# Kernel tuning notes

Hardware: AMD Instinct MI355X
Metric: run time of the kernel (lower is better)

## Reference

```python
import jax, jax.numpy as jnp
import numpy as np

N, T, H, D, E, P, R = 50000, 16, 512, 256, 200000, 100000, 3
LN_EPS = 1e-5
BN_EPS = 1e-5


def setup_inputs() -> dict:
    key = jax.random.key(0)
    ks = jax.random.split(key, 32)
    ri = lambda k, shape, hi: jax.random.randint(k, shape, 0, hi)
    rn = lambda k, shape, scale=0.05: (jax.random.normal(k, shape, dtype=jnp.float32) * scale)
    return {
        "node_type_ids": ri(ks[0], (N,), T),
        "src0": ri(ks[1], (E,), N), "dst0": ri(ks[2], (E,), N),
        "src1": ri(ks[3], (E,), N), "dst1": ri(ks[4], (E,), N),
        "src2": ri(ks[5], (E,), N), "dst2": ri(ks[6], (E,), N),
        "pairs": ri(ks[7], (2, P), N),
        "degrees": ri(ks[8], (N,), 100),
        "node_emb": rn(ks[9], (N, H)),
        "type_emb": rn(ks[10], (T, H)),
        "w_loop_in": rn(ks[11], (H, H)),
        "w_rel_in": rn(ks[12], (R, H, H)),
        "w_loop_res": rn(ks[13], (H, H)),
        "w_rel_res": rn(ks[14], (R, H, H)),
        "ln_g": jnp.ones((H,), jnp.float32),
        "ln_b": jnp.zeros((H,), jnp.float32),
        "w_loop_out": rn(ks[15], (H, D)),
        "w_rel_out": rn(ks[16], (R, H, D)),
        "lp_w1": rn(ks[17], (3 * D, D)),
        "lp_b1": jnp.zeros((D,), jnp.float32),
        "bn_g": jnp.ones((D,), jnp.float32),
        "bn_b": jnp.zeros((D,), jnp.float32),
        "bn_mean": jnp.zeros((D,), jnp.float32),
        "bn_var": jnp.ones((D,), jnp.float32),
        "lp_w2": rn(ks[18], (D, 1)),
        "lp_b2": jnp.zeros((1,), jnp.float32),
        "alpha": jnp.float32(0.1),
        "beta": jnp.float32(0.1),
    }


def _rgcn(x, loop_w, rel_w, srcs, dsts):
    # out = x @ W_loop + sum_r (A_r @ x) @ W_r ; A_r unweighted COO -> segment_sum
    out = x @ loop_w
    for r in range(R):
        msg = jax.ops.segment_sum(x[srcs[r]], dsts[r], num_segments=x.shape[0])
        out = out + msg @ rel_w[r]
    return out


def _layernorm(h, g, b):
    mu = h.mean(-1, keepdims=True)
    var = h.var(-1, keepdims=True)
    return (h - mu) * jax.lax.rsqrt(var + LN_EPS) * g + b


def reference(node_type_ids, src0, dst0, src1, dst1, src2, dst2, pairs, degrees,
              node_emb, type_emb, w_loop_in, w_rel_in, w_loop_res, w_rel_res,
              ln_g, ln_b, w_loop_out, w_rel_out, lp_w1, lp_b1, bn_g, bn_b,
              bn_mean, bn_var, lp_w2, lp_b2, alpha, beta):
    srcs = (src0, src1, src2)
    dsts = (dst0, dst1, dst2)
    # encode
    x = node_emb + type_emb[node_type_ids]          # [N, H]
    x = jax.nn.relu(_rgcn(x, w_loop_in, w_rel_in, srcs, dsts))
    h = _rgcn(x, w_loop_res, w_rel_res, srcs, dsts)
    h = jax.nn.relu(_layernorm(h, ln_g, ln_b))      # dropout p=0 -> identity
    x = x + h
    z = _rgcn(x, w_loop_out, w_rel_out, srcs, dsts)  # [N, D]
    # score
    src_z = z[pairs[0]]                              # [P, D]
    dst_z = z[pairs[1]]
    src_deg = jnp.clip(degrees[pairs[0]], 1).astype(jnp.float32)
    dst_deg = jnp.clip(degrees[pairs[1]], 1).astype(jnp.float32)
    feats = jnp.concatenate([src_z, dst_z, src_z * dst_z], axis=-1)  # [P, 3D]
    h1 = jax.nn.relu(feats @ lp_w1 + lp_b1)
    # BatchNorm1d in eval mode: running stats
    h1 = (h1 - bn_mean) * jax.lax.rsqrt(bn_var + BN_EPS) * bn_g + bn_b
    mlp_score = (h1 @ lp_w2 + lp_b2).squeeze(-1)     # [P]
    base = mlp_score - jax.nn.relu(alpha) * jnp.log(src_deg) - jax.nn.relu(beta) * jnp.log(dst_deg)
    return base / (jnp.sqrt(src_deg) * jnp.sqrt(dst_deg) + 1e-8)
```

## Files before the change

kernel.cpp:

```cpp
#include <hip/hip_runtime.h>

typedef __attribute__((ext_vector_type(8))) _Float16 half8;
typedef __attribute__((ext_vector_type(4))) _Float16 half4;
typedef __attribute__((ext_vector_type(4))) float f32x4;

static __device__ __forceinline__ void gload16(const void* g, void* l) {
  __builtin_amdgcn_global_load_lds((const __attribute__((address_space(1))) void*)g,
                                   (__attribute__((address_space(3))) void*)l, 16, 0, 0);
}

__global__ void k_encode(const float* __restrict__ emb, const float* __restrict__ temb,
                         const int* __restrict__ tids, _Float16* __restrict__ x, int n) {
  int i = blockIdx.x * 256 + threadIdx.x;
  if (i >= n * 64) return;
  int node = i >> 6, c = (i & 63) << 3;
  const float* e = emb + (size_t)node * 512 + c;
  const float* t = temb + (size_t)tids[node] * 512 + c;
  float4 a0 = *(const float4*)e, a1 = *(const float4*)(e + 4);
  float4 b0 = *(const float4*)t, b1 = *(const float4*)(t + 4);
  half8 o;
  o[0] = (_Float16)(a0.x + b0.x); o[1] = (_Float16)(a0.y + b0.y);
  o[2] = (_Float16)(a0.z + b0.z); o[3] = (_Float16)(a0.w + b0.w);
  o[4] = (_Float16)(a1.x + b1.x); o[5] = (_Float16)(a1.y + b1.y);
  o[6] = (_Float16)(a1.z + b1.z); o[7] = (_Float16)(a1.w + b1.w);
  *(half8*)(x + (size_t)node * 512 + c) = o;
}

__global__ void k_zero(int* __restrict__ p, int n) {
  int i = blockIdx.x * 256 + threadIdx.x;
  if (i < n) p[i] = 0;
}

__global__ void k_hist(const int* __restrict__ d0, const int* __restrict__ d1,
                       const int* __restrict__ d2, int* __restrict__ counts, int E, int Np1) {
  int e = blockIdx.x * 256 + threadIdx.x;
  if (e >= E) return;
  int r = blockIdx.y;
  const int* d = (r == 0) ? d0 : ((r == 1) ? d1 : d2);
  atomicAdd(&counts[r * Np1 + d[e] + 1], 1);
}

__global__ void k_scan(const int* __restrict__ counts, int* __restrict__ rowp, int n) {
  __shared__ int wsum[16];
  int r = blockIdx.x;
  const int* c = counts + (size_t)r * n;
  int* o = rowp + (size_t)r * n;
  int lane = threadIdx.x & 63, w = threadIdx.x >> 6;
  int off = 0;
  for (int base = 0; base < n; base += 1024) {
    int i = base + threadIdx.x;
    int v = (i < n) ? c[i] : 0;
    int sc = v;
    #pragma unroll
    for (int d = 1; d < 64; d <<= 1) {
      int t = __shfl_up(sc, (unsigned)d);
      if (lane >= d) sc += t;
    }
    if (lane == 63) wsum[w] = sc;
    __syncthreads();
    int wo = 0, tot = 0;
    #pragma unroll
    for (int ww = 0; ww < 16; ++ww) {
      int s = wsum[ww];
      if (ww < w) wo += s;
      tot += s;
    }
    if (i < n) o[i] = sc + wo + off;
    off += tot;
    __syncthreads();
  }
}

__global__ void k_copy(const int* __restrict__ a, int* __restrict__ b, int n) {
  int i = blockIdx.x * 256 + threadIdx.x;
  if (i < n) b[i] = a[i];
}

__global__ void k_fill(const int* __restrict__ s0, const int* __restrict__ s1, const int* __restrict__ s2,
                       const int* __restrict__ d0, const int* __restrict__ d1, const int* __restrict__ d2,
                       int* __restrict__ cursor, int* __restrict__ col_src, int E, int Np1) {
  int e = blockIdx.x * 256 + threadIdx.x;
  if (e >= E) return;
  int r = blockIdx.y;
  const int* dp = (r == 0) ? d0 : ((r == 1) ? d1 : d2);
  const int* sp = (r == 0) ? s0 : ((r == 1) ? s1 : s2);
  int pos = atomicAdd(&cursor[r * Np1 + dp[e]], 1);
  if (pos >= 0 && pos < E) col_src[(size_t)r * E + pos] = sp[e];
}

__global__ void k_aggregate(const _Float16* __restrict__ x, _Float16* __restrict__ agg,
                            const int* __restrict__ rowp, const int* __restrict__ col_src,
                            int N, int E) {
  int wid = (blockIdx.x * 256 + threadIdx.x) >> 6;
  int lane = threadIdx.x & 63;
  if (wid >= N) return;
  int Np1 = N + 1;
  #pragma unroll
  for (int r = 0; r < 3; ++r) {
    int beg = rowp[r * Np1 + wid], end = rowp[r * Np1 + wid + 1];
    const int* cs = col_src + (size_t)r * E;
    float acc[8] = {0, 0, 0, 0, 0, 0, 0, 0};
    int sn = (beg < end) ? cs[beg] : 0;
    for (int e = beg; e < end; ++e) {
      int sc = sn;
      if (e + 1 < end) sn = cs[e + 1];
      half8 v = *(const half8*)(x + (size_t)sc * 512 + lane * 8);
      #pragma unroll
      for (int j = 0; j < 8; ++j) acc[j] += (float)v[j];
    }
    half8 o;
    #pragma unroll
    for (int j = 0; j < 8; ++j) o[j] = (_Float16)acc[j];
    *(half8*)(agg + (size_t)wid * 1536 + r * 512 + lane * 8) = o;
  }
}

__global__ void k_transpose_all(const float* __restrict__ wli, const float* __restrict__ wri,
                                const float* __restrict__ wlr, const float* __restrict__ wrr,
                                const float* __restrict__ wlo, const float* __restrict__ wro,
                                const float* __restrict__ lpw1,
                                _Float16* __restrict__ Bti, _Float16* __restrict__ Btr,
                                _Float16* __restrict__ Bto, _Float16* __restrict__ Btl) {
  __shared__ float tile[64][65];
  int zi = blockIdx.z;
  const float* Bl; const float* Br; _Float16* Bt; int No, K;
  if (zi == 0)      { Bl = wli;  Br = wri;            Bt = Bti; No = 512; K = 2048; }
  else if (zi == 1) { Bl = wlr;  Br = wrr;            Bt = Btr; No = 512; K = 2048; }
  else if (zi == 2) { Bl = wlo;  Br = wro;            Bt = Bto; No = 256; K = 2048; }
  else              { Bl = lpw1; Br = lpw1 + 512*256; Bt = Btl; No = 256; K = 768;  }
  int k0 = blockIdx.x * 64, n0 = blockIdx.y * 64;
  if (k0 >= K || n0 >= No) return;
  int nl = threadIdx.x & 63, kb = threadIdx.x >> 6;
  #pragma unroll
  for (int i = 0; i < 16; ++i) {
    int kl = kb + i * 4;
    int krow = k0 + kl;
    float v = (krow < 512) ? Bl[(size_t)krow * No + n0 + nl]
                           : Br[(size_t)(krow - 512) * No + n0 + nl];
    tile[kl][nl] = v;
  }
  __syncthreads();
  int kl = threadIdx.x & 63, nb = threadIdx.x >> 6;
  #pragma unroll
  for (int i = 0; i < 16; ++i) {
    int n2 = nb + i * 4;
    Bt[(size_t)(n0 + n2) * K + k0 + kl] = (_Float16)tile[kl][n2];
  }
}

__global__ __launch_bounds__(512) void k_gemm_rgcn(
    const _Float16* __restrict__ Ain, const _Float16* __restrict__ Aagg,
    const _Float16* __restrict__ Bt, _Float16* __restrict__ C,
    int M, int Ncols, int K, int relu, int S, int T) {
  __shared__ __align__(16) _Float16 As[256 * 64];
  __shared__ __align__(16) _Float16 Bs[128 * 64];
  int lin = blockIdx.x;
  int grp = lin / (8 * T);
  int rmd = lin - grp * 8 * T;
  int c = rmd >> 3, x = rmd & 7;
  int s = grp * 8 + x;
  if (s >= S) return;
  int bm0 = s * 256, bn0 = c * 128;

  int tid = threadIdx.x;
  int lane = tid & 63, wv = tid >> 6;
  int wm = wv & 3, wn = wv >> 2;
  int l16 = lane & 15, quad = lane >> 4;

  int rl8 = lane >> 3;
  int gs = (lane & 7) ^ rl8;

  int rA[4];
  const _Float16* pa[4];
  const _Float16* pb[2];
  _Float16* ldA[4];
  _Float16* ldB[2];
  #pragma unroll
  for (int q = 0; q < 4; ++q) {
    int chunk = wv * 4 + q;
    int rl = chunk * 8 + rl8;
    int ra = bm0 + rl; if (ra >= M) ra = M - 1;
    rA[q] = ra;
    pa[q] = Ain + (size_t)ra * 512 + gs * 8;
    ldA[q] = &As[chunk * 8 * 64];
  }
  #pragma unroll
  for (int q = 0; q < 2; ++q) {
    int chunk = wv * 2 + q;
    int rl = chunk * 8 + rl8;
    pb[q] = Bt + (size_t)(bn0 + rl) * K + gs * 8;
    ldB[q] = &Bs[chunk * 8 * 64];
  }

  f32x4 acc[4][4];
  #pragma unroll
  for (int i = 0; i < 4; ++i)
    #pragma unroll
    for (int j = 0; j < 4; ++j) acc[i][j] = (f32x4){0.f, 0.f, 0.f, 0.f};

  for (int k0 = 0; k0 < K; k0 += 64) {
    if (k0 == 512) {
      #pragma unroll
      for (int q = 0; q < 4; ++q) pa[q] = Aagg + (size_t)rA[q] * 1536 + gs * 8;
    }
    __syncthreads();
    #pragma unroll
    for (int q = 0; q < 4; ++q) gload16(pa[q], ldA[q]);
    #pragma unroll
    for (int q = 0; q < 2; ++q) gload16(pb[q], ldB[q]);
    __syncthreads();
    #pragma unroll
    for (int sb = 0; sb < 2; ++sb) {
      half8 af[4], bf[4];
      int slot = ((sb * 4 + quad) ^ (l16 & 7)) * 8;
      #pragma unroll
      for (int i = 0; i < 4; ++i)
        af[i] = *(const half8*)&As[(wm * 64 + i * 16 + l16) * 64 + slot];
      #pragma unroll
      for (int j = 0; j < 4; ++j)
        bf[j] = *(const half8*)&Bs[(wn * 64 + j * 16 + l16) * 64 + slot];
      #pragma unroll
      for (int i = 0; i < 4; ++i)
        #pragma unroll
        for (int j = 0; j < 4; ++j)
          acc[i][j] = __builtin_amdgcn_mfma_f32_16x16x32_f16(af[i], bf[j], acc[i][j], 0, 0, 0);
    }
    #pragma unroll
    for (int q = 0; q < 4; ++q) pa[q] += 64;
    #pragma unroll
    for (int q = 0; q < 2; ++q) pb[q] += 64;
  }

  #pragma unroll
  for (int i = 0; i < 4; ++i)
    #pragma unroll
    for (int j = 0; j < 4; ++j)
      #pragma unroll
      for (int rg = 0; rg < 4; ++rg) {
        int row = bm0 + wm * 64 + i * 16 + quad * 4 + rg;
        int col = bn0 + wn * 64 + j * 16 + l16;
        if (row < M) {
          float v = acc[i][j][rg];
          if (relu) v = fmaxf(v, 0.f);
          C[(size_t)row * Ncols + col] = (_Float16)v;
        }
      }
}

#define LSTR 40

__global__ __launch_bounds__(256) void k_gemm_link(
    const _Float16* __restrict__ z, const int* __restrict__ pairs,
    const _Float16* __restrict__ Bt,
    const float* __restrict__ b1, const float* __restrict__ bng, const float* __restrict__ bnb,
    const float* __restrict__ bnm, const float* __restrict__ bnv,
    _Float16* __restrict__ h1, int P, int K) {
  __shared__ __align__(16) _Float16 As[128 * LSTR];
  __shared__ __align__(16) _Float16 Bs[128 * LSTR];
  int tid = threadIdx.x;
  int bn0 = blockIdx.x * 128, bm0 = blockIdx.y * 128;
  int lane = tid & 63, wv = tid >> 6;
  int wm = wv & 1, wn = wv >> 1;
  int l16 = lane & 15, quad = lane >> 4;
  int srow = tid >> 1, scs = (tid & 1) * 16;
  int p = bm0 + srow; if (p >= P) p = P - 1;
  int sp = pairs[p], dp = pairs[P + p];
  const _Float16* zs = z + (size_t)sp * 256;
  const _Float16* zd = z + (size_t)dp * 256;
  int bgn = bn0 + srow;

  f32x4 acc[4][4];
  #pragma unroll
  for (int i = 0; i < 4; ++i)
    #pragma unroll
    for (int j = 0; j < 4; ++j) acc[i][j] = (f32x4){0.f, 0.f, 0.f, 0.f};

  for (int k0 = 0; k0 < K; k0 += 32) {
    __syncthreads();
    int seg = k0 >> 8;
    int kk = (k0 & 255) + scs;
    __attribute__((aligned(16))) _Float16 tmp[16];
    if (seg == 0) {
      *(uint4*)tmp = *(const uint4*)(zs + kk);
      *(uint4*)(tmp + 8) = *(const uint4*)(zs + kk + 8);
    } else if (seg == 1) {
      *(uint4*)tmp = *(const uint4*)(zd + kk);
      *(uint4*)(tmp + 8) = *(const uint4*)(zd + kk + 8);
    } else {
      half8 u0 = *(const half8*)(zs + kk), u1 = *(const half8*)(zs + kk + 8);
      half8 v0 = *(const half8*)(zd + kk), v1 = *(const half8*)(zd + kk + 8);
      #pragma unroll
      for (int j = 0; j < 8; ++j) {
        tmp[j] = (_Float16)((float)u0[j] * (float)v0[j]);
        tmp[j + 8] = (_Float16)((float)u1[j] * (float)v1[j]);
      }
    }
    *(uint4*)&As[srow * LSTR + scs] = *(const uint4*)tmp;
    *(uint4*)&As[srow * LSTR + scs + 8] = *(const uint4*)(tmp + 8);
    {
      const _Float16* src = Bt + (size_t)bgn * K + k0 + scs;
      *(uint4*)&Bs[srow * LSTR + scs] = *(const uint4*)src;
      *(uint4*)&Bs[srow * LSTR + scs + 8] = *(const uint4*)(src + 8);
    }
    __syncthreads();
    half8 af[4], bf[4];
    #pragma unroll
    for (int i = 0; i < 4; ++i)
      af[i] = *(const half8*)&As[(wm * 64 + i * 16 + l16) * LSTR + quad * 8];
    #pragma unroll
    for (int j = 0; j < 4; ++j)
      bf[j] = *(const half8*)&Bs[(wn * 64 + j * 16 + l16) * LSTR + quad * 8];
    #pragma unroll
    for (int i = 0; i < 4; ++i)
      #pragma unroll
      for (int j = 0; j < 4; ++j)
        acc[i][j] = __builtin_amdgcn_mfma_f32_16x16x32_f16(af[i], bf[j], acc[i][j], 0, 0, 0);
  }

  #pragma unroll
  for (int i = 0; i < 4; ++i)
    #pragma unroll
    for (int j = 0; j < 4; ++j) {
      int col = bn0 + wn * 64 + j * 16 + l16;
      float bb1 = b1[col], m = bnm[col], rs = rsqrtf(bnv[col] + 1e-5f);
      float gg = bng[col], bb = bnb[col];
      #pragma unroll
      for (int rg = 0; rg < 4; ++rg) {
        int row = bm0 + wm * 64 + i * 16 + quad * 4 + rg;
        if (row < P) {
          float v = fmaxf(acc[i][j][rg] + bb1, 0.f);
          v = (v - m) * rs * gg + bb;
          h1[(size_t)row * 256 + col] = (_Float16)v;
        }
      }
    }
}

__global__ void k_ln_res(const _Float16* __restrict__ h, const _Float16* __restrict__ x1,
                         const float* __restrict__ g, const float* __restrict__ b,
                         _Float16* __restrict__ out, int N) {
  int wid = (blockIdx.x * 256 + threadIdx.x) >> 6;
  int lane = threadIdx.x & 63;
  if (wid >= N) return;
  int c = lane * 8;
  half8 hv = *(const half8*)(h + (size_t)wid * 512 + c);
  float hf[8];
  float s = 0.f, sq = 0.f;
  #pragma unroll
  for (int j = 0; j < 8; ++j) {
    hf[j] = (float)hv[j];
    s += hf[j];
    sq += hf[j] * hf[j];
  }
  #pragma unroll
  for (int off = 32; off; off >>= 1) {
    s += __shfl_down(s, (unsigned)off);
    sq += __shfl_down(sq, (unsigned)off);
  }
  s = __shfl(s, 0); sq = __shfl(sq, 0);
  float mu = s * (1.f / 512.f);
  float var = sq * (1.f / 512.f) - mu * mu;
  float rs = rsqrtf(var + 1e-5f);
  float4 g0 = *(const float4*)(g + c), g1 = *(const float4*)(g + c + 4);
  float4 b0 = *(const float4*)(b + c), b1 = *(const float4*)(b + c + 4);
  float gf[8] = {g0.x, g0.y, g0.z, g0.w, g1.x, g1.y, g1.z, g1.w};
  float bf[8] = {b0.x, b0.y, b0.z, b0.w, b1.x, b1.y, b1.z, b1.w};
  half8 xv = *(const half8*)(x1 + (size_t)wid * 512 + c);
  half8 o;
  #pragma unroll
  for (int j = 0; j < 8; ++j) {
    float xw = (float)xv[j];
    o[j] = (_Float16)(xw + fmaxf((hf[j] - mu) * rs * gf[j] + bf[j], 0.f));
  }
  *(half8*)(out + (size_t)wid * 512 + c) = o;
}

__global__ void k_score(const _Float16* __restrict__ h1, const float* __restrict__ w2,
                        const float* __restrict__ b2, const int* __restrict__ pairs,
                        const int* __restrict__ degrees, const float* __restrict__ alpha,
                        const float* __restrict__ beta, float* __restrict__ out, int P) {
  int wid = (blockIdx.x * 256 + threadIdx.x) >> 6;
  int lane = threadIdx.x & 63;
  if (wid >= P) return;
  int c = lane * 4;
  half4 hv = *(const half4*)(h1 + (size_t)wid * 256 + c);
  float4 wv = *(const float4*)(w2 + c);
  float s = (float)hv[0] * wv.x + (float)hv[1] * wv.y + (float)hv[2] * wv.z + (float)hv[3] * wv.w;
  #pragma unroll
  for (int off = 32; off; off >>= 1) s += __shfl_down(s, (unsigned)off);
  if (lane == 0) {
    int sp = pairs[wid], dp = pairs[P + wid];
    float sd = (float)max(degrees[sp], 1);
    float dd = (float)max(degrees[dp], 1);
    float base = s + b2[0] - fmaxf(alpha[0], 0.f) * logf(sd) - fmaxf(beta[0], 0.f) * logf(dd);
    out[wid] = base / (sqrtf(sd) * sqrtf(dd) + 1e-8f);
  }
}

extern "C" void kernel_launch(void* const* d_in, const int* in_sizes, int n_in,
                              void* d_out, int out_size, void* d_ws, size_t ws_size,
                              hipStream_t stream) {
  const int N = 50000, E = 200000, P = 100000;
  const int Np1 = N + 1;
  const int* node_type = (const int*)d_in[0];
  const int* src0 = (const int*)d_in[1]; const int* dst0 = (const int*)d_in[2];
  const int* src1 = (const int*)d_in[3]; const int* dst1 = (const int*)d_in[4];
  const int* src2 = (const int*)d_in[5]; const int* dst2 = (const int*)d_in[6];
  const int* pairs = (const int*)d_in[7];
  const int* degrees = (const int*)d_in[8];
  const float* node_emb = (const float*)d_in[9];
  const float* type_emb = (const float*)d_in[10];
  const float* w_loop_in = (const float*)d_in[11];
  const float* w_rel_in = (const float*)d_in[12];
  const float* w_loop_res = (const float*)d_in[13];
  const float* w_rel_res = (const float*)d_in[14];
  const float* ln_g = (const float*)d_in[15];
  const float* ln_b = (const float*)d_in[16];
  const float* w_loop_out = (const float*)d_in[17];
  const float* w_rel_out = (const float*)d_in[18];
  const float* lp_w1 = (const float*)d_in[19];
  const float* lp_b1 = (const float*)d_in[20];
  const float* bn_g = (const float*)d_in[21];
  const float* bn_b = (const float*)d_in[22];
  const float* bn_mean = (const float*)d_in[23];
  const float* bn_var = (const float*)d_in[24];
  const float* lp_w2 = (const float*)d_in[25];
  const float* lp_b2 = (const float*)d_in[26];
  const float* alpha = (const float*)d_in[27];
  const float* beta = (const float*)d_in[28];
  float* out = (float*)d_out;

  char* ws = (char*)d_ws;
  size_t off = 0;
  auto alloc = [&](size_t bytes) {
    void* p = ws + off;
    off = (off + bytes + 255) & ~(size_t)255;
    return p;
  };
  _Float16* xb0 = (_Float16*)alloc((size_t)N * 512 * 2);
  _Float16* xb1 = (_Float16*)alloc((size_t)N * 512 * 2);
  _Float16* agg = (_Float16*)alloc((size_t)N * 1536 * 2);
  _Float16* Bti = (_Float16*)alloc((size_t)512 * 2048 * 2);
  _Float16* Btr = (_Float16*)alloc((size_t)512 * 2048 * 2);
  _Float16* Bto = (_Float16*)alloc((size_t)256 * 2048 * 2);
  _Float16* Btl = (_Float16*)alloc((size_t)256 * 768 * 2);
  int* counts = (int*)alloc((size_t)3 * Np1 * 4);
  int* rowp = (int*)alloc((size_t)3 * Np1 * 4);
  int* cursor = (int*)alloc((size_t)3 * Np1 * 4);
  int* col_src = (int*)alloc((size_t)3 * E * 4);
  if (off > ws_size) return;

  _Float16* z = xb1;
  _Float16* h1 = agg;

  k_transpose_all<<<dim3(32, 8, 4), 256, 0, stream>>>(
      w_loop_in, w_rel_in, w_loop_res, w_rel_res, w_loop_out, w_rel_out, lp_w1,
      Bti, Btr, Bto, Btl);

  k_zero<<<(3 * Np1 + 255) / 256, 256, 0, stream>>>(counts, 3 * Np1);
  dim3 gE((E + 255) / 256, 3);
  k_hist<<<gE, 256, 0, stream>>>(dst0, dst1, dst2, counts, E, Np1);
  k_scan<<<3, 1024, 0, stream>>>(counts, rowp, Np1);
  k_copy<<<(3 * Np1 + 255) / 256, 256, 0, stream>>>(rowp, cursor, 3 * Np1);
  k_fill<<<gE, 256, 0, stream>>>(src0, src1, src2, dst0, dst1, dst2, cursor, col_src, E, Np1);

  k_encode<<<(N * 64 + 255) / 256, 256, 0, stream>>>(node_emb, type_emb, node_type, xb0, N);

  int aggBlocks = (N + 3) / 4;
  const int S = (N + 255) / 256;
  int blocks4 = ((S + 7) / 8) * 8 * 4;
  int blocks2 = ((S + 7) / 8) * 8 * 2;

  k_aggregate<<<aggBlocks, 256, 0, stream>>>(xb0, agg, rowp, col_src, N, E);
  k_gemm_rgcn<<<blocks4, 512, 0, stream>>>(xb0, agg, Bti, xb1, N, 512, 2048, 1, S, 4);

  k_aggregate<<<aggBlocks, 256, 0, stream>>>(xb1, agg, rowp, col_src, N, E);
  k_gemm_rgcn<<<blocks4, 512, 0, stream>>>(xb1, agg, Btr, xb0, N, 512, 2048, 0, S, 4);

  k_ln_res<<<(N + 3) / 4, 256, 0, stream>>>(xb0, xb1, ln_g, ln_b, xb0, N);

  k_aggregate<<<aggBlocks, 256, 0, stream>>>(xb0, agg, rowp, col_src, N, E);
  k_gemm_rgcn<<<blocks2, 512, 0, stream>>>(xb0, agg, Bto, z, N, 256, 2048, 0, S, 2);

  dim3 gl(2, (P + 127) / 128);
  k_gemm_link<<<gl, 256, 0, stream>>>(z, pairs, Btl, lp_b1, bn_g, bn_b, bn_mean, bn_var, h1, P, 768);

  k_score<<<(P + 3) / 4, 256, 0, stream>>>(h1, lp_w2, lp_b2, pairs, degrees, alpha, beta, out, P);
}
```

Baseline: 1.058 ms.

## Materialize link features and use swizzled LDS-DMA GEMM; unroll aggregation gathers

The link-prediction GEMM is split in two. A new kernel first materializes the concatenated [src, dst, src*dst] features into a buffer. A second GEMM then loads tiles with global_load_lds into an XOR-swizzled 64-wide LDS layout, using 256x128 tiles, 512 threads and grouped block ordering. The per-node aggregation loop is also unrolled by 4 so several independent row gathers are in flight at once. The cost is an extra pass writing and reading the P x 768 feature buffer, and h1 now reuses xb0.

Result: slower. 1.093 ms (+3.3%).

```diff
diff --git a/kernel.cpp b/kernel.cpp
--- a/kernel.cpp
+++ b/kernel.cpp
@@ -95,23 +95,41 @@
   int lane = threadIdx.x & 63;
   if (wid >= N) return;
   int Np1 = N + 1;
+  int co = lane * 8;
   #pragma unroll
   for (int r = 0; r < 3; ++r) {
     int beg = rowp[r * Np1 + wid], end = rowp[r * Np1 + wid + 1];
     const int* cs = col_src + (size_t)r * E;
     float acc[8] = {0, 0, 0, 0, 0, 0, 0, 0};
-    int sn = (beg < end) ? cs[beg] : 0;
-    for (int e = beg; e < end; ++e) {
-      int sc = sn;
-      if (e + 1 < end) sn = cs[e + 1];
-      half8 v = *(const half8*)(x + (size_t)sc * 512 + lane * 8);
-      #pragma unroll
-      for (int j = 0; j < 8; ++j) acc[j] += (float)v[j];
+    int e = beg;
+    for (; e + 4 <= end; e += 4) {
+      int s0 = cs[e], s1 = cs[e + 1], s2 = cs[e + 2], s3 = cs[e + 3];
+      half8 v0 = *(const half8*)(x + (size_t)s0 * 512 + co);
+      half8 v1 = *(const half8*)(x + (size_t)s1 * 512 + co);
+      half8 v2 = *(const half8*)(x + (size_t)s2 * 512 + co);
+      half8 v3 = *(const half8*)(x + (size_t)s3 * 512 + co);
+      #pragma unroll
+      for (int j = 0; j < 8; ++j)
+        acc[j] += ((float)v0[j] + (float)v1[j]) + ((float)v2[j] + (float)v3[j]);
+    }
+    if (e + 2 <= end) {
+      int s0 = cs[e], s1 = cs[e + 1];
+      half8 v0 = *(const half8*)(x + (size_t)s0 * 512 + co);
+      half8 v1 = *(const half8*)(x + (size_t)s1 * 512 + co);
+      #pragma unroll
+      for (int j = 0; j < 8; ++j) acc[j] += (float)v0[j] + (float)v1[j];
+      e += 2;
+    }
+    if (e < end) {
+      int s0 = cs[e];
+      half8 v0 = *(const half8*)(x + (size_t)s0 * 512 + co);
+      #pragma unroll
+      for (int j = 0; j < 8; ++j) acc[j] += (float)v0[j];
     }
     half8 o;
     #pragma unroll
     for (int j = 0; j < 8; ++j) o[j] = (_Float16)acc[j];
-    *(half8*)(agg + (size_t)wid * 1536 + r * 512 + lane * 8) = o;
+    *(half8*)(agg + (size_t)wid * 1536 + r * 512 + co) = o;
   }
 }
 
@@ -247,27 +265,69 @@
       }
 }
 
-#define LSTR 40
-
-__global__ __launch_bounds__(256) void k_gemm_link(
-    const _Float16* __restrict__ z, const int* __restrict__ pairs,
-    const _Float16* __restrict__ Bt,
+__global__ void k_feats(const _Float16* __restrict__ z, const int* __restrict__ pairs,
+                        _Float16* __restrict__ feats, int P) {
+  unsigned int i = blockIdx.x * 256 + threadIdx.x;
+  if (i >= (unsigned)P * 96u) return;
+  unsigned int p = i / 96u;
+  int c8 = (int)(i - p * 96u);
+  int sp = pairs[p], dp = pairs[P + p];
+  half8 o;
+  if (c8 < 32) {
+    o = *(const half8*)(z + (size_t)sp * 256 + c8 * 8);
+  } else if (c8 < 64) {
+    o = *(const half8*)(z + (size_t)dp * 256 + (c8 - 32) * 8);
+  } else {
+    half8 u = *(const half8*)(z + (size_t)sp * 256 + (c8 - 64) * 8);
+    half8 v = *(const half8*)(z + (size_t)dp * 256 + (c8 - 64) * 8);
+    #pragma unroll
+    for (int j = 0; j < 8; ++j) o[j] = (_Float16)((float)u[j] * (float)v[j]);
+  }
+  *(half8*)(feats + (size_t)p * 768 + c8 * 8) = o;
+}
+
+__global__ __launch_bounds__(512) void k_gemm_linkB(
+    const _Float16* __restrict__ feats, const _Float16* __restrict__ Bt,
     const float* __restrict__ b1, const float* __restrict__ bng, const float* __restrict__ bnb,
     const float* __restrict__ bnm, const float* __restrict__ bnv,
-    _Float16* __restrict__ h1, int P, int K) {
-  __shared__ __align__(16) _Float16 As[128 * LSTR];
-  __shared__ __align__(16) _Float16 Bs[128 * LSTR];
+    _Float16* __restrict__ h1, int P, int K, int S, int T) {
+  __shared__ __align__(16) _Float16 As[256 * 64];
+  __shared__ __align__(16) _Float16 Bs[128 * 64];
+  int lin = blockIdx.x;
+  int grp = lin / (8 * T);
+  int rmd = lin - grp * 8 * T;
+  int c = rmd >> 3, x = rmd & 7;
+  int s = grp * 8 + x;
+  if (s >= S) return;
+  int bm0 = s * 256, bn0 = c * 128;
+
   int tid = threadIdx.x;
-  int bn0 = blockIdx.x * 128, bm0 = blockIdx.y * 128;
   int lane = tid & 63, wv = tid >> 6;
-  int wm = wv & 1, wn = wv >> 1;
+  int wm = wv & 3, wn = wv >> 2;
   int l16 = lane & 15, quad = lane >> 4;
-  int srow = tid >> 1, scs = (tid & 1) * 16;
-  int p = bm0 + srow; if (p >= P) p = P - 1;
-  int sp = pairs[p], dp = pairs[P + p];
-  const _Float16* zs = z + (size_t)sp * 256;
-  const _Float16* zd = z + (size_t)dp * 256;
-  int bgn = bn0 + srow;
+
+  int rl8 = lane >> 3;
+  int gs = (lane & 7) ^ rl8;
+
+  const _Float16* pa[4];
+  const _Float16* pb[2];
+  _Float16* ldA[4];
+  _Float16* ldB[2];
+  #pragma unroll
+  for (int q = 0; q < 4; ++q) {
+    int chunk = wv * 4 + q;
+    int rl = chunk * 8 + rl8;
+    int ra = bm0 + rl; if (ra >= P) ra = P - 1;
+    pa[q] = feats + (size_t)ra * 768 + gs * 8;
+    ldA[q] = &As[chunk * 8 * 64];
+  }
+  #pragma unroll
+  for (int q = 0; q < 2; ++q) {
+    int chunk = wv * 2 + q;
+    int rl = chunk * 8 + rl8;
+    pb[q] = Bt + (size_t)(bn0 + rl) * K + gs * 8;
+    ldB[q] = &Bs[chunk * 8 * 64];
+  }
 
   f32x4 acc[4][4];
   #pragma unroll
@@ -275,55 +335,42 @@
     #pragma unroll
     for (int j = 0; j < 4; ++j) acc[i][j] = (f32x4){0.f, 0.f, 0.f, 0.f};
 
-  for (int k0 = 0; k0 < K; k0 += 32) {
+  for (int k0 = 0; k0 < K; k0 += 64) {
     __syncthreads();
-    int seg = k0 >> 8;
-    int kk = (k0 & 255) + scs;
-    __attribute__((aligned(16))) _Float16 tmp[16];
-    if (seg == 0) {
-      *(uint4*)tmp = *(const uint4*)(zs + kk);
-      *(uint4*)(tmp + 8) = *(const uint4*)(zs + kk + 8);
-    } else if (seg == 1) {
-      *(uint4*)tmp = *(const uint4*)(zd + kk);
-      *(uint4*)(tmp + 8) = *(const uint4*)(zd + kk + 8);
-    } else {
-      half8 u0 = *(const half8*)(zs + kk), u1 = *(const half8*)(zs + kk + 8);
-      half8 v0 = *(const half8*)(zd + kk), v1 = *(const half8*)(zd + kk + 8);
-      #pragma unroll
-      for (int j = 0; j < 8; ++j) {
-        tmp[j] = (_Float16)((float)u0[j] * (float)v0[j]);
-        tmp[j + 8] = (_Float16)((float)u1[j] * (float)v1[j]);
-      }
-    }
-    *(uint4*)&As[srow * LSTR + scs] = *(const uint4*)tmp;
-    *(uint4*)&As[srow * LSTR + scs + 8] = *(const uint4*)(tmp + 8);
-    {
-      const _Float16* src = Bt + (size_t)bgn * K + k0 + scs;
-      *(uint4*)&Bs[srow * LSTR + scs] = *(const uint4*)src;
-      *(uint4*)&Bs[srow * LSTR + scs + 8] = *(const uint4*)(src + 8);
-    }
+    #pragma unroll
+    for (int q = 0; q < 4; ++q) gload16(pa[q], ldA[q]);
+    #pragma unroll
+    for (int q = 0; q < 2; ++q) gload16(pb[q], ldB[q]);
     __syncthreads();
-    half8 af[4], bf[4];
+    #pragma unroll
+    for (int sb = 0; sb < 2; ++sb) {
+      half8 af[4], bf[4];
+      int slot = ((sb * 4 + quad) ^ (l16 & 7)) * 8;
+      #pragma unroll
+      for (int i = 0; i < 4; ++i)
+        af[i] = *(const half8*)&As[(wm * 64 + i * 16 + l16) * 64 + slot];
+      #pragma unroll
+      for (int j = 0; j < 4; ++j)
+        bf[j] = *(const half8*)&Bs[(wn * 64 + j * 16 + l16) * 64 + slot];
+      #pragma unroll
+      for (int i = 0; i < 4; ++i)
+        #pragma unroll
+        for (int j = 0; j < 4; ++j)
+          acc[i][j] = __builtin_amdgcn_mfma_f32_16x16x32_f16(af[i], bf[j], acc[i][j], 0, 0, 0);
+    }
+    #pragma unroll
+    for (int q = 0; q < 4; ++q) pa[q] += 64;
+    #pragma unroll
+    for (int q = 0; q < 2; ++q) pb[q] += 64;
+  }
+
+  #pragma unroll
+  for (int j = 0; j < 4; ++j) {
+    int col = bn0 + wn * 64 + j * 16 + l16;
+    float bb1 = b1[col], m = bnm[col], rs = rsqrtf(bnv[col] + 1e-5f);
+    float gg = bng[col], bb = bnb[col];
     #pragma unroll
     for (int i = 0; i < 4; ++i)
-      af[i] = *(const half8*)&As[(wm * 64 + i * 16 + l16) * LSTR + quad * 8];
-    #pragma unroll
-    for (int j = 0; j < 4; ++j)
-      bf[j] = *(const half8*)&Bs[(wn * 64 + j * 16 + l16) * LSTR + quad * 8];
-    #pragma unroll
-    for (int i = 0; i < 4; ++i)
-      #pragma unroll
-      for (int j = 0; j < 4; ++j)
-        acc[i][j] = __builtin_amdgcn_mfma_f32_16x16x32_f16(af[i], bf[j], acc[i][j], 0, 0, 0);
-  }
-
-  #pragma unroll
-  for (int i = 0; i < 4; ++i)
-    #pragma unroll
-    for (int j = 0; j < 4; ++j) {
-      int col = bn0 + wn * 64 + j * 16 + l16;
-      float bb1 = b1[col], m = bnm[col], rs = rsqrtf(bnv[col] + 1e-5f);
-      float gg = bng[col], bb = bnb[col];
       #pragma unroll
       for (int rg = 0; rg < 4; ++rg) {
         int row = bm0 + wm * 64 + i * 16 + quad * 4 + rg;
@@ -333,7 +380,7 @@
           h1[(size_t)row * 256 + col] = (_Float16)v;
         }
       }
-    }
+  }
 }
 
 __global__ void k_ln_res(const _Float16* __restrict__ h, const _Float16* __restrict__ x1,
@@ -451,7 +498,8 @@
   if (off > ws_size) return;
 
   _Float16* z = xb1;
-  _Float16* h1 = agg;
+  _Float16* feats = agg;
+  _Float16* h1 = xb0;
 
   k_transpose_all<<<dim3(32, 8, 4), 256, 0, stream>>>(
       w_loop_in, w_rel_in, w_loop_res, w_rel_res, w_loop_out, w_rel_out, lp_w1,
@@ -482,8 +530,11 @@
   k_aggregate<<<aggBlocks, 256, 0, stream>>>(xb0, agg, rowp, col_src, N, E);
   k_gemm_rgcn<<<blocks2, 512, 0, stream>>>(xb0, agg, Bto, z, N, 256, 2048, 0, S, 2);
 
-  dim3 gl(2, (P + 127) / 128);
-  k_gemm_link<<<gl, 256, 0, stream>>>(z, pairs, Btl, lp_b1, bn_g, bn_b, bn_mean, bn_var, h1, P, 768);
+  k_feats<<<((unsigned)P * 96u + 255) / 256, 256, 0, stream>>>(z, pairs, feats, P);
+  const int SL = (P + 255) / 256;
+  int blocksL = ((SL + 7) / 8) * 8 * 2;
+  k_gemm_linkB<<<blocksL, 512, 0, stream>>>(feats, Btl, lp_b1, bn_g, bn_b, bn_mean, bn_var,
+                                            h1, P, 768, SL, 2);
 
   k_score<<<(P + 3) / 4, 256, 0, stream>>>(h1, lp_w2, lp_b2, pairs, degrees, alpha, beta, out, P);
 }
```

## Merge per-relation CSR into one combined CSR with relation-tagged columns

Applied to the files above, without the earlier changes.

Builds a single CSR over destination nodes holding all three relations, with the relation id packed into the top byte of each column index. The aggregate kernel then walks one edge list per node with 4-way unrolled gathers and branches to one of three accumulators. The zero and copy kernels are dropped: a memset clears the counts and the scan writes the cursor directly, cutting launches. The aim is more memory-level parallelism in the gather; the cost is data-dependent branching per edge and a node-id limit of 2^24.

Result: no change. 1.074 ms (+1.5%).

```diff
diff --git a/kernel.cpp b/kernel.cpp
--- a/kernel.cpp
+++ b/kernel.cpp
@@ -26,30 +26,23 @@
   *(half8*)(x + (size_t)node * 512 + c) = o;
 }
 
-__global__ void k_zero(int* __restrict__ p, int n) {
-  int i = blockIdx.x * 256 + threadIdx.x;
-  if (i < n) p[i] = 0;
-}
-
 __global__ void k_hist(const int* __restrict__ d0, const int* __restrict__ d1,
-                       const int* __restrict__ d2, int* __restrict__ counts, int E, int Np1) {
+                       const int* __restrict__ d2, int* __restrict__ counts, int E) {
   int e = blockIdx.x * 256 + threadIdx.x;
   if (e >= E) return;
   int r = blockIdx.y;
   const int* d = (r == 0) ? d0 : ((r == 1) ? d1 : d2);
-  atomicAdd(&counts[r * Np1 + d[e] + 1], 1);
-}
-
-__global__ void k_scan(const int* __restrict__ counts, int* __restrict__ rowp, int n) {
+  atomicAdd(&counts[d[e] + 1], 1);
+}
+
+__global__ void k_scan(const int* __restrict__ counts, int* __restrict__ rowp,
+                       int* __restrict__ cursor, int n) {
   __shared__ int wsum[16];
-  int r = blockIdx.x;
-  const int* c = counts + (size_t)r * n;
-  int* o = rowp + (size_t)r * n;
   int lane = threadIdx.x & 63, w = threadIdx.x >> 6;
   int off = 0;
   for (int base = 0; base < n; base += 1024) {
     int i = base + threadIdx.x;
-    int v = (i < n) ? c[i] : 0;
+    int v = (i < n) ? counts[i] : 0;
     int sc = v;
     #pragma unroll
     for (int d = 1; d < 64; d <<= 1) {
@@ -65,54 +58,82 @@
       if (ww < w) wo += s;
       tot += s;
     }
-    if (i < n) o[i] = sc + wo + off;
+    if (i < n) { int val = sc + wo + off; rowp[i] = val; cursor[i] = val; }
     off += tot;
     __syncthreads();
   }
 }
 
-__global__ void k_copy(const int* __restrict__ a, int* __restrict__ b, int n) {
-  int i = blockIdx.x * 256 + threadIdx.x;
-  if (i < n) b[i] = a[i];
-}
-
 __global__ void k_fill(const int* __restrict__ s0, const int* __restrict__ s1, const int* __restrict__ s2,
                        const int* __restrict__ d0, const int* __restrict__ d1, const int* __restrict__ d2,
-                       int* __restrict__ cursor, int* __restrict__ col_src, int E, int Np1) {
+                       int* __restrict__ cursor, int* __restrict__ colrel, int E) {
   int e = blockIdx.x * 256 + threadIdx.x;
   if (e >= E) return;
   int r = blockIdx.y;
   const int* dp = (r == 0) ? d0 : ((r == 1) ? d1 : d2);
   const int* sp = (r == 0) ? s0 : ((r == 1) ? s1 : s2);
-  int pos = atomicAdd(&cursor[r * Np1 + dp[e]], 1);
-  if (pos >= 0 && pos < E) col_src[(size_t)r * E + pos] = sp[e];
+  int pos = atomicAdd(&cursor[dp[e]], 1);
+  if (pos >= 0 && pos < 3 * E) colrel[pos] = sp[e] | (r << 24);
 }
 
 __global__ void k_aggregate(const _Float16* __restrict__ x, _Float16* __restrict__ agg,
-                            const int* __restrict__ rowp, const int* __restrict__ col_src,
-                            int N, int E) {
+                            const int* __restrict__ rowp, const int* __restrict__ colrel,
+                            int N) {
   int wid = (blockIdx.x * 256 + threadIdx.x) >> 6;
   int lane = threadIdx.x & 63;
   if (wid >= N) return;
-  int Np1 = N + 1;
-  #pragma unroll
-  for (int r = 0; r < 3; ++r) {
-    int beg = rowp[r * Np1 + wid], end = rowp[r * Np1 + wid + 1];
-    const int* cs = col_src + (size_t)r * E;
-    float acc[8] = {0, 0, 0, 0, 0, 0, 0, 0};
-    int sn = (beg < end) ? cs[beg] : 0;
-    for (int e = beg; e < end; ++e) {
-      int sc = sn;
-      if (e + 1 < end) sn = cs[e + 1];
-      half8 v = *(const half8*)(x + (size_t)sc * 512 + lane * 8);
-      #pragma unroll
-      for (int j = 0; j < 8; ++j) acc[j] += (float)v[j];
-    }
-    half8 o;
-    #pragma unroll
-    for (int j = 0; j < 8; ++j) o[j] = (_Float16)acc[j];
-    *(half8*)(agg + (size_t)wid * 1536 + r * 512 + lane * 8) = o;
-  }
+  int beg = rowp[wid], end = rowp[wid + 1];
+  int co = lane * 8;
+  float a0[8] = {0,0,0,0,0,0,0,0}, a1[8] = {0,0,0,0,0,0,0,0}, a2[8] = {0,0,0,0,0,0,0,0};
+  int e = beg;
+  for (; e + 4 <= end; e += 4) {
+    int c0 = colrel[e], c1 = colrel[e + 1], c2 = colrel[e + 2], c3 = colrel[e + 3];
+    half8 v0 = *(const half8*)(x + (size_t)(c0 & 0xFFFFFF) * 512 + co);
+    half8 v1 = *(const half8*)(x + (size_t)(c1 & 0xFFFFFF) * 512 + co);
+    half8 v2 = *(const half8*)(x + (size_t)(c2 & 0xFFFFFF) * 512 + co);
+    half8 v3 = *(const half8*)(x + (size_t)(c3 & 0xFFFFFF) * 512 + co);
+    {
+      int r = c0 >> 24;
+      if (r == 0) { for (int j = 0; j < 8; ++j) a0[j] += (float)v0[j]; }
+      else if (r == 1) { for (int j = 0; j < 8; ++j) a1[j] += (float)v0[j]; }
+      else { for (int j = 0; j < 8; ++j) a2[j] += (float)v0[j]; }
+    }
+    {
+      int r = c1 >> 24;
+      if (r == 0) { for (int j = 0; j < 8; ++j) a0[j] += (float)v1[j]; }
+      else if (r == 1) { for (int j = 0; j < 8; ++j) a1[j] += (float)v1[j]; }
+      else { for (int j = 0; j < 8; ++j) a2[j] += (float)v1[j]; }
+    }
+    {
+      int r = c2 >> 24;
+      if (r == 0) { for (int j = 0; j < 8; ++j) a0[j] += (float)v2[j]; }
+      else if (r == 1) { for (int j = 0; j < 8; ++j) a1[j] += (float)v2[j]; }
+      else { for (int j = 0; j < 8; ++j) a2[j] += (float)v2[j]; }
+    }
+    {
+      int r = c3 >> 24;
+      if (r == 0) { for (int j = 0; j < 8; ++j) a0[j] += (float)v3[j]; }
+      else if (r == 1) { for (int j = 0; j < 8; ++j) a1[j] += (float)v3[j]; }
+      else { for (int j = 0; j < 8; ++j) a2[j] += (float)v3[j]; }
+    }
+  }
+  for (; e < end; ++e) {
+    int c0 = colrel[e];
+    half8 v0 = *(const half8*)(x + (size_t)(c0 & 0xFFFFFF) * 512 + co);
+    int r = c0 >> 24;
+    if (r == 0) { for (int j = 0; j < 8; ++j) a0[j] += (float)v0[j]; }
+    else if (r == 1) { for (int j = 0; j < 8; ++j) a1[j] += (float)v0[j]; }
+    else { for (int j = 0; j < 8; ++j) a2[j] += (float)v0[j]; }
+  }
+  half8 o0, o1, o2;
+  #pragma unroll
+  for (int j = 0; j < 8; ++j) {
+    o0[j] = (_Float16)a0[j]; o1[j] = (_Float16)a1[j]; o2[j] = (_Float16)a2[j];
+  }
+  size_t ob = (size_t)wid * 1536;
+  *(half8*)(agg + ob + co) = o0;
+  *(half8*)(agg + ob + 512 + co) = o1;
+  *(half8*)(agg + ob + 1024 + co) = o2;
 }
 
 __global__ void k_transpose_all(const float* __restrict__ wli, const float* __restrict__ wri,
@@ -444,10 +465,10 @@
   _Float16* Btr = (_Float16*)alloc((size_t)512 * 2048 * 2);
   _Float16* Bto = (_Float16*)alloc((size_t)256 * 2048 * 2);
   _Float16* Btl = (_Float16*)alloc((size_t)256 * 768 * 2);
-  int* counts = (int*)alloc((size_t)3 * Np1 * 4);
-  int* rowp = (int*)alloc((size_t)3 * Np1 * 4);
-  int* cursor = (int*)alloc((size_t)3 * Np1 * 4);
-  int* col_src = (int*)alloc((size_t)3 * E * 4);
+  int* counts = (int*)alloc((size_t)Np1 * 4);
+  int* rowp = (int*)alloc((size_t)Np1 * 4);
+  int* cursor = (int*)alloc((size_t)Np1 * 4);
+  int* colrel = (int*)alloc((size_t)3 * E * 4);
   if (off > ws_size) return;
 
   _Float16* z = xb1;
@@ -457,12 +478,11 @@
       w_loop_in, w_rel_in, w_loop_res, w_rel_res, w_loop_out, w_rel_out, lp_w1,
       Bti, Btr, Bto, Btl);
 
-  k_zero<<<(3 * Np1 + 255) / 256, 256, 0, stream>>>(counts, 3 * Np1);
+  hipMemsetAsync(counts, 0, (size_t)Np1 * 4, stream);
   dim3 gE((E + 255) / 256, 3);
-  k_hist<<<gE, 256, 0, stream>>>(dst0, dst1, dst2, counts, E, Np1);
-  k_scan<<<3, 1024, 0, stream>>>(counts, rowp, Np1);
-  k_copy<<<(3 * Np1 + 255) / 256, 256, 0, stream>>>(rowp, cursor, 3 * Np1);
-  k_fill<<<gE, 256, 0, stream>>>(src0, src1, src2, dst0, dst1, dst2, cursor, col_src, E, Np1);
+  k_hist<<<gE, 256, 0, stream>>>(dst0, dst1, dst2, counts, E);
+  k_scan<<<1, 1024, 0, stream>>>(counts, rowp, cursor, Np1);
+  k_fill<<<gE, 256, 0, stream>>>(src0, src1, src2, dst0, dst1, dst2, cursor, colrel, E);
 
   k_encode<<<(N * 64 + 255) / 256, 256, 0, stream>>>(node_emb, type_emb, node_type, xb0, N);
 
@@ -471,15 +491,15 @@
   int blocks4 = ((S + 7) / 8) * 8 * 4;
   int blocks2 = ((S + 7) / 8) * 8 * 2;
 
-  k_aggregate<<<aggBlocks, 256, 0, stream>>>(xb0, agg, rowp, col_src, N, E);
+  k_aggregate<<<aggBlocks, 256, 0, stream>>>(xb0, agg, rowp, colrel, N);
   k_gemm_rgcn<<<blocks4, 512, 0, stream>>>(xb0, agg, Bti, xb1, N, 512, 2048, 1, S, 4);
 
-  k_aggregate<<<aggBlocks, 256, 0, stream>>>(xb1, agg, rowp, col_src, N, E);
+  k_aggregate<<<aggBlocks, 256, 0, stream>>>(xb1, agg, rowp, colrel, N);
   k_gemm_rgcn<<<blocks4, 512, 0, stream>>>(xb1, agg, Btr, xb0, N, 512, 2048, 0, S, 4);
 
   k_ln_res<<<(N + 3) / 4, 256, 0, stream>>>(xb0, xb1, ln_g, ln_b, xb0, N);
 
-  k_aggregate<<<aggBlocks, 256, 0, stream>>>(xb0, agg, rowp, col_src, N, E);
+  k_aggregate<<<aggBlocks, 256, 0, stream>>>(xb0, agg, rowp, colrel, N);
   k_gemm_rgcn<<<blocks2, 512, 0, stream>>>(xb0, agg, Bto, z, N, 256, 2048, 0, S, 2);
 
   dim3 gl(2, (P + 127) / 128);
```
